# Kernel optimization log

Measured on AMD Instinct MI355X. Metric: run time of the kernel, lower is better.

The kernel has to match this reference:

```python
import jax, jax.numpy as jnp
import numpy as np

NBINS = 30
LO, HI = -6.0, 6.0
BINWIDTH = (HI - LO) / (NBINS - 2)  # interior bin width, matches abs((hi-lo)/(nbins-2))


def setup_inputs() -> dict:
    key = jax.random.key(0)
    x = jax.random.normal(key, (4096, 16384), dtype=jnp.float32)
    return {"x": x}


def reference(x):
    # Single-pass digitize + scatter-add, mathematically identical to the
    # original per-bin threshold-compare loop:
    #   bin 0 (orig BinPop[1]):      x <  LO
    #   bin i (orig BinPop[i+1]):    LO+(i-1)*w <= x < LO+i*w, i=1..nbins-2
    #   bin nbins-1 (BinPop[nbins]): x >= HI   (HI == LO + (nbins-2)*w)
    b, n = x.shape
    k = jnp.clip(jnp.floor((x - LO) / BINWIDTH), -1.0, NBINS - 2).astype(jnp.int32) + 1
    rows = jnp.arange(b, dtype=jnp.int32)[:, None]  # [b,1] broadcast against [b,n]
    hist_nat = jnp.zeros((b, NBINS), dtype=x.dtype).at[rows, k].add(1.0)
    # The original concatenates dict values in insertion order:
    # [bin1, bin_nbins, bin2, ..., bin_{nbins-1}]
    order = np.concatenate([[0], [NBINS - 1], np.arange(1, NBINS - 1)])
    return hist_nat[:, order]
```

## Files before the change

kernel.cpp:

```cpp
#include <hip/hip_runtime.h>


#define NBINS   30
#define STRIDE  33
#define THREADS 256
#define ROWLEN  16384
#define ITERS   (ROWLEN / 4 / THREADS)

__global__ __launch_bounds__(THREADS, 4) void hist_kernel(
    const float* __restrict__ x, float* __restrict__ out)
{
    __shared__ unsigned int h[THREADS * STRIDE];
    __shared__ unsigned int partial[8 * NBINS];

    const int t   = threadIdx.x;
    const int row = blockIdx.x;

    unsigned int* hp = &h[t * STRIDE];
#pragma unroll
    for (int i = 0; i < STRIDE; ++i) hp[i] = 0u;
    __syncthreads();

    const float W    = (float)(12.0 / 28.0);
    const float invW = 1.0f / W;

    const float4* xr = (const float4*)(x + (size_t)row * ROWLEN);

#pragma unroll
    for (int i = 0; i < ITERS; ++i) {
        float4 v = xr[t + i * THREADS];
        {
            int k = __float2int_rd((v.x + 6.0f) * invW);
            k = min(max(k, -1), NBINS - 2) + 1;
            atomicAdd(&hp[k], 1u);
        }
        {
            int k = __float2int_rd((v.y + 6.0f) * invW);
            k = min(max(k, -1), NBINS - 2) + 1;
            atomicAdd(&hp[k], 1u);
        }
        {
            int k = __float2int_rd((v.z + 6.0f) * invW);
            k = min(max(k, -1), NBINS - 2) + 1;
            atomicAdd(&hp[k], 1u);
        }
        {
            int k = __float2int_rd((v.w + 6.0f) * invW);
            k = min(max(k, -1), NBINS - 2) + 1;
            atomicAdd(&hp[k], 1u);
        }
    }
    __syncthreads();

    if (t < 240) {
        const int bin = t % NBINS;
        const int g   = t / NBINS;
        unsigned int s = 0;
        const int c0 = g * 32;
#pragma unroll
        for (int c = 0; c < 32; ++c)
            s += h[(c0 + c) * STRIDE + bin];
        partial[g * NBINS + bin] = s;
    }
    __syncthreads();

    if (t < NBINS) {
        unsigned int s = 0;
#pragma unroll
        for (int g = 0; g < 8; ++g) s += partial[g * NBINS + t];
        const int dst = (t == 0) ? 0 : (t == NBINS - 1) ? 1 : (t + 1);
        out[(size_t)row * NBINS + dst] = (float)s;
    }
}

extern "C" void kernel_launch(void* const* d_in, const int* in_sizes, int n_in,
                              void* d_out, int out_size, void* d_ws, size_t ws_size,
                              hipStream_t stream)
{
    const float* x  = (const float*)d_in[0];
    float* out      = (float*)d_out;
    const int rows  = in_sizes[0] / ROWLEN;
    hist_kernel<<<rows, THREADS, 0, stream>>>(x, out);
}
```

Baseline: 351.2 us.

## Transpose per-thread LDS histograms to bin-major layout and use nontemporal loads

```diff
diff --git a/kernel.cpp b/kernel.cpp
--- a/kernel.cpp
+++ b/kernel.cpp
@@ -2,65 +2,66 @@
 
 
 #define NBINS   30
-#define STRIDE  33
 #define THREADS 256
 #define ROWLEN  16384
 #define ITERS   (ROWLEN / 4 / THREADS)
 
+typedef float f4 __attribute__((ext_vector_type(4)));
+
 __global__ __launch_bounds__(THREADS, 4) void hist_kernel(
     const float* __restrict__ x, float* __restrict__ out)
 {
-    __shared__ unsigned int h[THREADS * STRIDE];
+    __shared__ unsigned int h[NBINS * THREADS];
     __shared__ unsigned int partial[8 * NBINS];
 
     const int t   = threadIdx.x;
     const int row = blockIdx.x;
 
-    unsigned int* hp = &h[t * STRIDE];
 #pragma unroll
-    for (int i = 0; i < STRIDE; ++i) hp[i] = 0u;
+    for (int b = 0; b < NBINS; ++b) h[b * THREADS + t] = 0u;
     __syncthreads();
 
     const float W    = (float)(12.0 / 28.0);
     const float invW = 1.0f / W;
+    const float c6   = 6.0f * invW;
 
-    const float4* xr = (const float4*)(x + (size_t)row * ROWLEN);
+    const f4* xr = (const f4*)(x + (size_t)row * ROWLEN);
+    const int base = THREADS + t;
 
 #pragma unroll
     for (int i = 0; i < ITERS; ++i) {
-        float4 v = xr[t + i * THREADS];
+        f4 v = __builtin_nontemporal_load(&xr[t + i * THREADS]);
         {
-            int k = __float2int_rd((v.x + 6.0f) * invW);
-            k = min(max(k, -1), NBINS - 2) + 1;
-            atomicAdd(&hp[k], 1u);
+            int k = __float2int_rd(fmaf(v.x, invW, c6));
+            k = min(max(k, -1), NBINS - 2);
+            atomicAdd(&h[k * THREADS + base], 1u);
         }
         {
-            int k = __float2int_rd((v.y + 6.0f) * invW);
-            k = min(max(k, -1), NBINS - 2) + 1;
-            atomicAdd(&hp[k], 1u);
+            int k = __float2int_rd(fmaf(v.y, invW, c6));
+            k = min(max(k, -1), NBINS - 2);
+            atomicAdd(&h[k * THREADS + base], 1u);
         }
         {
-            int k = __float2int_rd((v.z + 6.0f) * invW);
-            k = min(max(k, -1), NBINS - 2) + 1;
-            atomicAdd(&hp[k], 1u);
+            int k = __float2int_rd(fmaf(v.z, invW, c6));
+            k = min(max(k, -1), NBINS - 2);
+            atomicAdd(&h[k * THREADS + base], 1u);
         }
         {
-            int k = __float2int_rd((v.w + 6.0f) * invW);
-            k = min(max(k, -1), NBINS - 2) + 1;
-            atomicAdd(&hp[k], 1u);
+            int k = __float2int_rd(fmaf(v.w, invW, c6));
+            k = min(max(k, -1), NBINS - 2);
+            atomicAdd(&h[k * THREADS + base], 1u);
         }
     }
     __syncthreads();
 
     if (t < 240) {
-        const int bin = t % NBINS;
-        const int g   = t / NBINS;
+        const int b = t % NBINS;
+        const int g = t / NBINS;
         unsigned int s = 0;
-        const int c0 = g * 32;
 #pragma unroll
-        for (int c = 0; c < 32; ++c)
-            s += h[(c0 + c) * STRIDE + bin];
-        partial[g * NBINS + bin] = s;
+        for (int i = 0; i < 32; ++i)
+            s += h[b * THREADS + g * 32 + ((i + b) & 31)];
+        partial[g * NBINS + b] = s;
     }
     __syncthreads();
 
```

New measurement: 334.6 us. 4.7% less time.
